# Performance work log

Measured on AMD Instinct MI355X. Metric: run time of the kernel, lower is better.

## Reference

```python
import jax, jax.numpy as jnp
import numpy as np

N_NODES = 100000
N_EDGES = 1600000
F_IN = 128
HIDDEN = [128, 128]
F_OUT = 64


def _glorot(key, shape):
    fan_in, fan_out = shape[1], shape[0]
    lim = jnp.sqrt(6.0 / (fan_in + fan_out))
    return jax.random.uniform(key, shape, jnp.float32, -lim, lim)


def setup_inputs() -> dict:
    key = jax.random.key(0)
    ks = jax.random.split(key, 12)
    x = jax.random.normal(ks[0], (N_NODES, F_IN), jnp.float32)
    edge_index = jax.random.randint(ks[1], (2, N_EDGES), 0, N_NODES, jnp.int64)
    dims = [F_IN] + HIDDEN + [F_OUT]  # [128, 128, 128, 64]
    inp = {"x": x, "edge_index": edge_index}
    for i in range(3):
        din, dout = dims[i], dims[i + 1]
        inp[f"Wl{i}"] = _glorot(ks[2 + 3 * i], (dout, din))  # neighbor lin (lin_l)
        inp[f"Wr{i}"] = _glorot(ks[3 + 3 * i], (dout, din))  # root lin (lin_r)
        inp[f"b{i}"] = jnp.zeros((dout,), jnp.float32)
    return inp


def sage_conv(x, src, dst, Wl, Wr, b):
    # PyG SAGEConv, aggr='mean': out = lin_l(mean_{j in N(i)} x_j) + lin_r(x_i) + bias
    msg = x[src]  # [E, Fin] gather from source nodes
    agg = jax.ops.segment_sum(msg, dst, num_segments=N_NODES)  # [N, Fin]
    deg = jax.ops.segment_sum(jnp.ones((src.shape[0],), x.dtype), dst,
                              num_segments=N_NODES)  # [N]
    mean = agg / jnp.maximum(deg, 1.0)[:, None]
    return mean @ Wl.T + x @ Wr.T + b


def reference(x, edge_index, Wl0, Wr0, b0, Wl1, Wr1, b1, Wl2, Wr2, b2):
    src, dst = edge_index[0], edge_index[1]
    h = jax.nn.relu(sage_conv(x, src, dst, Wl0, Wr0, b0))
    h = jax.nn.relu(sage_conv(h, src, dst, Wl1, Wr1, b1))
    out = sage_conv(h, src, dst, Wl2, Wr2, b2)  # final_conv: no relu
    return out
```

## Files before the change

kernel.cpp:

```cpp
#include <hip/hip_runtime.h>

#define NF 128
#define CHUNK 8192

typedef __attribute__((ext_vector_type(8))) short bf16x8;
typedef __attribute__((ext_vector_type(4))) float f32x4;
typedef __attribute__((ext_vector_type(2))) float f32x2;

__device__ __forceinline__ unsigned short f2b(float f) {
    unsigned int u = __float_as_uint(f);
    unsigned int r = (u + 0x7fffu + ((u >> 16) & 1u)) >> 16;
    return (unsigned short)r;
}

__device__ __forceinline__ void gld_lds16(const void* g, const void* l) {
    __builtin_amdgcn_global_load_lds(
        (const __attribute__((address_space(1))) unsigned int*)(unsigned long long)g,
        (__attribute__((address_space(3))) unsigned int*)(unsigned int)(unsigned long long)l,
        16, 0, 0);
}


__global__ __launch_bounds__(256) void prep_kernel(
        const float* __restrict__ x, unsigned short* __restrict__ xb,
        unsigned char* __restrict__ x8, int n4,
        const float* __restrict__ Wl0, const float* __restrict__ Wr0, unsigned short* __restrict__ Wc0,
        const float* __restrict__ Wl1, const float* __restrict__ Wr1, unsigned short* __restrict__ Wc1,
        const float* __restrict__ Wl2, const float* __restrict__ Wr2, const float* __restrict__ b2,
        unsigned short* __restrict__ Wst, float* __restrict__ bst,
        const int* __restrict__ dst, int* __restrict__ hist, int E, int NB,
        int bCvt, int bW0, int bW1, int bWs) {
    __shared__ int hsh[512];
    const int blk = blockIdx.x;
    const int tid = threadIdx.x;
    if (blk < bCvt) {
        int i = blk * 256 + tid;
        if (i < n4) {
            float4 v = *(const float4*)&x[(size_t)i * 4];
            uint2 o;
            o.x = (unsigned int)f2b(v.x) | ((unsigned int)f2b(v.y) << 16);
            o.y = (unsigned int)f2b(v.z) | ((unsigned int)f2b(v.w) << 16);
            *(uint2*)&xb[(size_t)i * 4] = o;
            unsigned p = __builtin_amdgcn_cvt_pk_fp8_f32(v.x, v.y, 0, false);
            p = __builtin_amdgcn_cvt_pk_fp8_f32(v.z, v.w, p, true);
            *(unsigned int*)&x8[(size_t)i * 4] = p;
        }
    } else if (blk < bW1) {
        const bool first = blk < bW0;
        int i = (blk - (first ? bCvt : bW0)) * 256 + tid;
        const float* Wl = first ? Wl0 : Wl1;
        const float* Wr = first ? Wr0 : Wr1;
        unsigned short* Wc = first ? Wc0 : Wc1;
        int f = i >> 7, k = i & 127;
        Wc[f * 256 + k] = f2b(Wl[i]);
        Wc[f * 256 + 128 + k] = f2b(Wr[i]);
    } else if (blk < bWs) {
        int i = (blk - bW1) * 256 + tid;
        int f = i >> 7, k = i & 127;
        Wst[f * 128 + k] = f2b(Wl2[i]);
        Wst[(f + 64) * 128 + k] = f2b(Wr2[i]);
        if (k == 0) {
            bst[f] = 0.f;
            bst[f + 64] = b2[f];
        }
    } else {
        const int hb = blk - bWs;
        for (int i = tid; i < NB; i += 256) hsh[i] = 0;
        __syncthreads();
        const int e0 = hb * CHUNK;
        for (int i = tid; i < CHUNK; i += 256) {
            int e = e0 + i;
            if (e < E) atomicAdd(&hsh[dst[e] >> 8], 1);
        }
        __syncthreads();
        for (int i = tid; i < NB; i += 256) hist[hb * NB + i] = hsh[i];
    }
}


__global__ __launch_bounds__(256) void sb_sum(const int* __restrict__ hist,
                                              int* __restrict__ bsum,
                                              int T, int NB, int NBLK) {
    int i = blockIdx.x * 256 + threadIdx.x;
    int v = 0;
    if (i < T) {
        int b = i / NBLK, blk = i - b * NBLK;
        v = hist[blk * NB + b];
    }
#pragma unroll
    for (int d = 32; d; d >>= 1) v += __shfl_down(v, d, 64);
    __shared__ int wsum[4];
    if ((threadIdx.x & 63) == 0) wsum[threadIdx.x >> 6] = v;
    __syncthreads();
    if (threadIdx.x == 0) bsum[blockIdx.x] = wsum[0] + wsum[1] + wsum[2] + wsum[3];
}

__global__ __launch_bounds__(1024) void sb_scan(const int* __restrict__ bsum,
                                                int* __restrict__ bpre, int NS) {
    __shared__ int s[1024];
    int t = threadIdx.x;
    int v = (t < NS) ? bsum[t] : 0;
    s[t] = v;
    __syncthreads();
    for (int d = 1; d < 1024; d <<= 1) {
        int u = (t >= d) ? s[t - d] : 0;
        __syncthreads();
        s[t] += u;
        __syncthreads();
    }
    if (t < NS) bpre[t] = s[t] - v;
}

__global__ __launch_bounds__(256) void sb_apply(const int* __restrict__ hist,
                                                const int* __restrict__ bpre,
                                                int* __restrict__ base,
                                                int* __restrict__ bstart,
                                                int T, int NB, int NBLK, int E) {
    __shared__ int s[256];
    int i = blockIdx.x * 256 + threadIdx.x;
    int t = threadIdx.x;
    int v = 0;
    int b = 0, blk = 0;
    if (i < T) {
        b = i / NBLK;
        blk = i - b * NBLK;
        v = hist[blk * NB + b];
    }
    s[t] = v;
    __syncthreads();
    for (int d = 1; d < 256; d <<= 1) {
        int u = (t >= d) ? s[t - d] : 0;
        __syncthreads();
        s[t] += u;
        __syncthreads();
    }
    if (i < T) {
        int val = bpre[blockIdx.x] + s[t] - v;
        base[i] = val;
        if (blk == 0) bstart[b] = val;
        if (i == 0) bstart[NB] = E;
    }
}

__global__ __launch_bounds__(256) void scat_kernel(const int* __restrict__ src,
                                                   const int* __restrict__ dst,
                                                   const int* __restrict__ base,
                                                   unsigned int* __restrict__ recs,
                                                   int E, int NB, int NBLK) {
    __shared__ int cur[512];
    const int blk = blockIdx.x;
    for (int b = threadIdx.x; b < NB; b += 256) cur[b] = base[b * NBLK + blk];
    __syncthreads();
    const int e0 = blk * CHUNK;
    for (int i = threadIdx.x; i < CHUNK; i += 256) {
        int e = e0 + i;
        if (e >= E) continue;
        int d = dst[e];
        int b = d >> 8;
        int pos = atomicAdd(&cur[b], 1);
        recs[pos] = (unsigned int)src[e] | ((unsigned int)(d & 255) << 24);
    }
}

__global__ __launch_bounds__(256) void csr_kernel(const unsigned int* __restrict__ recs,
                                                  const int* __restrict__ bstart,
                                                  int* __restrict__ offs,
                                                  float* __restrict__ rdeg,
                                                  int* __restrict__ csr,
                                                  int N, int E) {
    __shared__ int cnt[256];
    __shared__ int sc[256];
    __shared__ int cur[256];
    const int b = blockIdx.x;
    const int t = threadIdx.x;
    const int s0 = bstart[b], s1 = bstart[b + 1];
    cnt[t] = 0;
    __syncthreads();
    for (int i = s0 + t; i < s1; i += 256) atomicAdd(&cnt[recs[i] >> 24], 1);
    __syncthreads();
    int v = cnt[t];
    sc[t] = v;
    __syncthreads();
    for (int d = 1; d < 256; d <<= 1) {
        int u = (t >= d) ? sc[t - d] : 0;
        __syncthreads();
        sc[t] += u;
        __syncthreads();
    }
    int excl = sc[t] - v;
    int node = b * 256 + t;
    if (node < N) {
        offs[node] = s0 + excl;
        rdeg[node] = 1.0f / (float)(v > 1 ? v : 1);
        if (node == N - 1) offs[N] = E;
    }
    cur[t] = s0 + excl;
    __syncthreads();
    for (int i = s0 + t; i < s1; i += 256) {
        unsigned int r = recs[i];
        int pos = atomicAdd(&cur[r >> 24], 1);
        csr[pos] = (int)(r & 0xFFFFFFu);
    }
}


__global__ __launch_bounds__(256) void agg8_kernel(
        const unsigned char* __restrict__ h8, const int* __restrict__ offs,
        const int* __restrict__ csr, const float* __restrict__ rdeg,
        unsigned short* __restrict__ meanout, int N) {
    const int node = blockIdx.x * 4 + (threadIdx.x >> 6);
    const int lane = threadIdx.x & 63;
    if (node >= N) return;
    const int s0 = offs[node], s1 = offs[node + 1];
    const char* __restrict__ hb = (const char*)h8;
    const unsigned lane2 = (unsigned)lane * 2u;
    f32x2 acc = {0.f, 0.f};
    for (int base = s0; base < s1; base += 64) {
        const int cnt = min(64, s1 - base);
        const int boff = csr[base + min(lane, cnt - 1)] << 7;
        int j = 0;
#define AGG8_GROUP(NG)                                                         \
        {                                                                      \
            unsigned o[NG];                                                    \
            _Pragma("unroll")                                                  \
            for (int k = 0; k < NG; ++k)                                       \
                o[k] = (unsigned)__shfl(boff, j + k, 64) + lane2;              \
            unsigned int v[NG];                                                \
            _Pragma("unroll")                                                  \
            for (int k = 0; k < NG; ++k)                                       \
                v[k] = *(const unsigned short*)(hb + o[k]);                    \
            _Pragma("unroll")                                                  \
            for (int k = 0; k < NG; ++k)                                       \
                acc += __builtin_amdgcn_cvt_pk_f32_fp8(v[k], false);           \
            j += NG;                                                           \
        }
        while (j + 16 <= cnt) AGG8_GROUP(16)
        if (cnt & 8) AGG8_GROUP(8)
        if (cnt & 4) AGG8_GROUP(4)
        if (cnt & 2) AGG8_GROUP(2)
        if (cnt & 1) AGG8_GROUP(1)
#undef AGG8_GROUP
    }
    float r = rdeg[node];
    unsigned int o = (unsigned int)f2b(acc.x * r) | ((unsigned int)f2b(acc.y * r) << 16);
    *(unsigned int*)&meanout[(size_t)node * NF + lane * 2] = o;
}


__global__ __launch_bounds__(256) void agg2_kernel(
        const unsigned short* __restrict__ z, const int* __restrict__ offs,
        const int* __restrict__ csr, const float* __restrict__ rdeg,
        float* __restrict__ out, int N) {
    const int node = blockIdx.x * 4 + (threadIdx.x >> 6);
    const int lane = threadIdx.x & 63;
    if (node >= N) return;
    const int s0 = offs[node], s1 = offs[node + 1];
    const char* __restrict__ zb = (const char*)z;
    const unsigned lane2 = (unsigned)lane * 2u;
    float acc = 0.f;
    for (int base = s0; base < s1; base += 64) {
        const int cnt = min(64, s1 - base);
        const int boff = csr[base + min(lane, cnt - 1)] << 8;
        int j = 0;
#define AGG2_GROUP(NG)                                                         \
        {                                                                      \
            unsigned o[NG];                                                    \
            _Pragma("unroll")                                                  \
            for (int k = 0; k < NG; ++k)                                       \
                o[k] = (unsigned)__shfl(boff, j + k, 64) + lane2;              \
            unsigned int v[NG];                                                \
            _Pragma("unroll")                                                  \
            for (int k = 0; k < NG; ++k)                                       \
                v[k] = *(const unsigned short*)(zb + o[k]);                    \
            _Pragma("unroll")                                                  \
            for (int k = 0; k < NG; ++k)                                       \
                acc += __uint_as_float(v[k] << 16);                            \
            j += NG;                                                           \
        }
        while (j + 16 <= cnt) AGG2_GROUP(16)
        if (cnt & 8) AGG2_GROUP(8)
        if (cnt & 4) AGG2_GROUP(4)
        if (cnt & 2) AGG2_GROUP(2)
        if (cnt & 1) AGG2_GROUP(1)
#undef AGG2_GROUP
    }
    float r = rdeg[node];
    unsigned int vr = *(const unsigned short*)(zb + (size_t)node * 256 + 128 + lane2);
    out[(size_t)node * 64 + lane] = acc * r + __uint_as_float(vr << 16);
}


template <bool OUT8>
__global__ __launch_bounds__(256) void gemm_kernel(
        const unsigned short* __restrict__ Abuf,
        const unsigned short* __restrict__ Hbuf,
        const unsigned short* __restrict__ Wcat,
        const float* __restrict__ bias,
        unsigned short* __restrict__ outb,
        unsigned char* __restrict__ out8,
        int N) {
    __shared__ unsigned short As[64 * 256];

    const int tid = threadIdx.x, wid = tid >> 6, lane = tid & 63;
    const int m0 = blockIdx.x * 64;
    char* Ac = (char*)As;
    const char* Ab = (const char*)Abuf;
    const char* Hb = (const char*)Hbuf;
    const char* Wb = (const char*)Wcat;

#pragma unroll
    for (int i = 0; i < 8; ++i) {
        int off = wid * 8192 + i * 1024 + lane * 16;
        int row = off >> 9, c = off & 511;
        int c2 = c ^ ((row & 7) << 4);
        const char* srcp = (c2 < 256) ? (Ab + (size_t)(m0 + row) * 256 + c2)
                                      : (Hb + (size_t)(m0 + row) * 256 + (c2 - 256));
        gld_lds16(srcp, Ac + wid * 8192 + i * 1024);
    }
    asm volatile("s_waitcnt vmcnt(0)" ::: "memory");
    __syncthreads();

    constexpr int MI = 2;
    constexpr int NI = 4;
    const int lm = lane & 15, ko = lane >> 4;
    const int wmBase = (wid >> 1) * 32;
    const int wnBase = (wid & 1) * 64;

    f32x4 acc[MI][NI];
#pragma unroll
    for (int i = 0; i < MI; ++i)
#pragma unroll
        for (int j = 0; j < NI; ++j)
            acc[i][j] = (f32x4){0.f, 0.f, 0.f, 0.f};

#pragma unroll
    for (int ks = 0; ks < 8; ++ks) {
        const int kb = ks * 64 + ko * 16;
        bf16x8 a[MI], b[NI];
#pragma unroll
        for (int j = 0; j < NI; ++j) {
            int row = wnBase + j * 16 + lm;
            b[j] = *(const bf16x8*)(Wb + row * 512 + kb);
        }
#pragma unroll
        for (int i = 0; i < MI; ++i) {
            int row = wmBase + i * 16 + lm;
            a[i] = *(const bf16x8*)(Ac + row * 512 + (kb ^ ((row & 7) << 4)));
        }
#pragma unroll
        for (int i = 0; i < MI; ++i)
#pragma unroll
            for (int j = 0; j < NI; ++j)
                acc[i][j] = __builtin_amdgcn_mfma_f32_16x16x32_bf16(b[j], a[i], acc[i][j], 0, 0, 0);
    }

#pragma unroll
    for (int i = 0; i < MI; ++i) {
        const int node = m0 + wmBase + i * 16 + lm;
        if (node < N) {
#pragma unroll
            for (int j = 0; j < NI; ++j) {
                const int col0 = wnBase + j * 16 + ko * 4;
                const float4 bv = *(const float4*)&bias[col0];
                float v0 = fmaxf(acc[i][j][0] + bv.x, 0.f);
                float v1 = fmaxf(acc[i][j][1] + bv.y, 0.f);
                float v2 = fmaxf(acc[i][j][2] + bv.z, 0.f);
                float v3 = fmaxf(acc[i][j][3] + bv.w, 0.f);
                uint2 o;
                o.x = (unsigned int)f2b(v0) | ((unsigned int)f2b(v1) << 16);
                o.y = (unsigned int)f2b(v2) | ((unsigned int)f2b(v3) << 16);
                *(uint2*)&outb[(size_t)node * 128 + col0] = o;
                if (OUT8) {
                    unsigned p = __builtin_amdgcn_cvt_pk_fp8_f32(v0, v1, 0, false);
                    p = __builtin_amdgcn_cvt_pk_fp8_f32(v2, v3, p, true);
                    *(unsigned int*)&out8[(size_t)node * 128 + col0] = p;
                }
            }
        }
    }
}


__global__ __launch_bounds__(256) void gemmz_kernel(
        const unsigned short* __restrict__ A,
        const unsigned short* __restrict__ W,
        const float* __restrict__ bias,
        unsigned short* __restrict__ outb,
        int N) {
    __shared__ unsigned short As[64 * 128];

    const int tid = threadIdx.x, wid = tid >> 6, lane = tid & 63;
    const int m0 = blockIdx.x * 64;
    char* Ac = (char*)As;
    const char* Ab = (const char*)A;
    const char* Wb = (const char*)W;

#pragma unroll
    for (int i = 0; i < 4; ++i) {
        int off = wid * 4096 + i * 1024 + lane * 16;
        int row = off >> 8, c = off & 255;
        int c2 = c ^ ((row & 7) << 4);
        gld_lds16(Ab + (size_t)(m0 + row) * 256 + c2, Ac + wid * 4096 + i * 1024);
    }
    asm volatile("s_waitcnt vmcnt(0)" ::: "memory");
    __syncthreads();

    constexpr int MI = 2;
    constexpr int NI = 4;
    const int lm = lane & 15, ko = lane >> 4;
    const int wmBase = (wid >> 1) * 32;
    const int wnBase = (wid & 1) * 64;

    f32x4 acc[MI][NI];
#pragma unroll
    for (int i = 0; i < MI; ++i)
#pragma unroll
        for (int j = 0; j < NI; ++j)
            acc[i][j] = (f32x4){0.f, 0.f, 0.f, 0.f};

#pragma unroll
    for (int ks = 0; ks < 4; ++ks) {
        const int kb = ks * 64 + ko * 16;
        bf16x8 a[MI], b[NI];
#pragma unroll
        for (int j = 0; j < NI; ++j) {
            int row = wnBase + j * 16 + lm;
            b[j] = *(const bf16x8*)(Wb + row * 256 + kb);
        }
#pragma unroll
        for (int i = 0; i < MI; ++i) {
            int row = wmBase + i * 16 + lm;
            a[i] = *(const bf16x8*)(Ac + row * 256 + (kb ^ ((row & 7) << 4)));
        }
#pragma unroll
        for (int i = 0; i < MI; ++i)
#pragma unroll
            for (int j = 0; j < NI; ++j)
                acc[i][j] = __builtin_amdgcn_mfma_f32_16x16x32_bf16(b[j], a[i], acc[i][j], 0, 0, 0);
    }

#pragma unroll
    for (int i = 0; i < MI; ++i) {
        const int node = m0 + wmBase + i * 16 + lm;
        if (node < N) {
#pragma unroll
            for (int j = 0; j < NI; ++j) {
                const int col0 = wnBase + j * 16 + ko * 4;
                const float4 bv = *(const float4*)&bias[col0];
                uint2 o;
                o.x = (unsigned int)f2b(acc[i][j][0] + bv.x) |
                      ((unsigned int)f2b(acc[i][j][1] + bv.y) << 16);
                o.y = (unsigned int)f2b(acc[i][j][2] + bv.z) |
                      ((unsigned int)f2b(acc[i][j][3] + bv.w) << 16);
                *(uint2*)&outb[(size_t)node * 128 + col0] = o;
            }
        }
    }
}


extern "C" void kernel_launch(void* const* d_in, const int* in_sizes, int n_in,
                              void* d_out, int out_size, void* d_ws, size_t ws_size,
                              hipStream_t stream) {
    const float* x   = (const float*)d_in[0];
    const int*   ei  = (const int*)d_in[1];
    const float* Wl0 = (const float*)d_in[2];
    const float* Wr0 = (const float*)d_in[3];
    const float* b0  = (const float*)d_in[4];
    const float* Wl1 = (const float*)d_in[5];
    const float* Wr1 = (const float*)d_in[6];
    const float* b1  = (const float*)d_in[7];
    const float* Wl2 = (const float*)d_in[8];
    const float* Wr2 = (const float*)d_in[9];
    const float* b2  = (const float*)d_in[10];
    float* out = (float*)d_out;

    const int N = in_sizes[0] / NF;
    const int E = in_sizes[1] / 2;
    const int* srcv = ei;
    const int* dstv = ei + E;

    const int NB   = (N + 255) >> 8;
    const int NBLK = (E + CHUNK - 1) / CHUNK;
    const int T    = NB * NBLK;
    const int NS   = (T + 255) / 256;

    char* w = (char*)d_ws;
    auto alloc = [&](size_t bytes) {
        void* p = (void*)w;
        w += (bytes + 255) & ~(size_t)255;
        return p;
    };
    unsigned short* xb   = (unsigned short*)alloc((size_t)N * NF * 2);
    unsigned short* h1b  = (unsigned short*)alloc((size_t)N * NF * 2);
    unsigned short* h2b  = (unsigned short*)alloc((size_t)N * NF * 2);
    unsigned short* mb   = (unsigned short*)alloc((size_t)N * NF * 2);
    unsigned char*  u8   = (unsigned char*)alloc((size_t)N * NF * 2);
    unsigned char*  x8   = u8;
    unsigned char*  h18  = u8 + (size_t)N * NF;
    unsigned short* z2b  = (unsigned short*)u8;
    unsigned short* Wc0  = (unsigned short*)alloc((size_t)128 * 256 * 2);
    unsigned short* Wc1  = (unsigned short*)alloc((size_t)128 * 256 * 2);
    unsigned short* Wst2 = (unsigned short*)alloc((size_t)128 * 128 * 2);
    float*          bst2 = (float*)alloc((size_t)128 * 4);
    int*   offs   = (int*)alloc((size_t)(N + 1) * 4);
    int*   csr    = (int*)alloc((size_t)E * 4);
    float* rdeg   = (float*)alloc((size_t)N * 4);
    unsigned int* recs = (unsigned int*)alloc((size_t)E * 4);
    int*   hist   = (int*)alloc((size_t)T * 4);
    int*   base   = (int*)alloc((size_t)T * 4);
    int*   bstart = (int*)alloc((size_t)(NB + 1) * 4);
    int*   sb1    = (int*)alloc((size_t)1024 * 4);
    int*   sb2    = (int*)alloc((size_t)1024 * 4);

    const int n4 = N * NF / 4;
    const int bCvt = (n4 + 255) / 256;
    const int bW0  = bCvt + 64;
    const int bW1  = bW0 + 64;
    const int bWs  = bW1 + 32;
    const int bTot = bWs + NBLK;

    prep_kernel<<<bTot, 256, 0, stream>>>(x, xb, x8, n4,
                                          Wl0, Wr0, Wc0, Wl1, Wr1, Wc1,
                                          Wl2, Wr2, b2, Wst2, bst2,
                                          dstv, hist, E, NB,
                                          bCvt, bW0, bW1, bWs);
    sb_sum<<<NS, 256, 0, stream>>>(hist, sb1, T, NB, NBLK);
    sb_scan<<<1, 1024, 0, stream>>>(sb1, sb2, NS);
    sb_apply<<<NS, 256, 0, stream>>>(hist, sb2, base, bstart, T, NB, NBLK, E);
    scat_kernel<<<NBLK, 256, 0, stream>>>(srcv, dstv, base, recs, E, NB, NBLK);
    csr_kernel<<<NB, 256, 0, stream>>>(recs, bstart, offs, rdeg, csr, N, E);

    const int ab = (N + 3) / 4;
    const int gb = (N + 63) / 64;

    agg8_kernel<<<ab, 256, 0, stream>>>(x8, offs, csr, rdeg, mb, N);
    gemm_kernel<true><<<gb, 256, 0, stream>>>(mb, xb, Wc0, b0, h1b, h18, N);

    agg8_kernel<<<ab, 256, 0, stream>>>(h18, offs, csr, rdeg, mb, N);
    gemm_kernel<false><<<gb, 256, 0, stream>>>(mb, h1b, Wc1, b1, h2b, nullptr, N);

    gemmz_kernel<<<gb, 256, 0, stream>>>(h2b, Wst2, bst2, z2b, N);
    agg2_kernel<<<ab, 256, 0, stream>>>(z2b, offs, csr, rdeg, out, N);
}
```

Before: 306.6 us.

## Fuse mean aggregation into the layer GEMM via shared-memory tiles

Measured after the change: 346.0 us. 1.13x slower.

```diff
diff --git a/kernel.cpp b/kernel.cpp
--- a/kernel.cpp
+++ b/kernel.cpp
@@ -204,46 +204,139 @@
 }
 
 
-__global__ __launch_bounds__(256) void agg8_kernel(
-        const unsigned char* __restrict__ h8, const int* __restrict__ offs,
-        const int* __restrict__ csr, const float* __restrict__ rdeg,
-        unsigned short* __restrict__ meanout, int N) {
-    const int node = blockIdx.x * 4 + (threadIdx.x >> 6);
-    const int lane = threadIdx.x & 63;
-    if (node >= N) return;
-    const int s0 = offs[node], s1 = offs[node + 1];
-    const char* __restrict__ hb = (const char*)h8;
+template <bool OUT8>
+__global__ __launch_bounds__(256) void fused_layer(
+        const unsigned char* __restrict__ g8,
+        const unsigned short* __restrict__ root,
+        const int* __restrict__ offs, const int* __restrict__ csr,
+        const float* __restrict__ rdeg,
+        const unsigned short* __restrict__ Wcat,
+        const float* __restrict__ bias,
+        unsigned short* __restrict__ outb,
+        unsigned char* __restrict__ out8,
+        int N) {
+    __shared__ unsigned short Am[64 * 128];
+    __shared__ unsigned short Ar[64 * 128];
+
+    const int tid = threadIdx.x, wid = tid >> 6, lane = tid & 63;
+    const int m0 = blockIdx.x * 64;
+    char* Amc = (char*)Am;
+    char* Arc = (char*)Ar;
+    const char* Rb = (const char*)root;
+    const char* Wb = (const char*)Wcat;
+
+#pragma unroll
+    for (int i = 0; i < 4; ++i) {
+        int off = wid * 4096 + i * 1024 + lane * 16;
+        int row = off >> 8, c = off & 255;
+        int c2 = c ^ ((row & 7) << 4);
+        gld_lds16(Rb + (size_t)(m0 + row) * 256 + c2, Arc + wid * 4096 + i * 1024);
+    }
+
+    const char* __restrict__ hb = (const char*)g8;
     const unsigned lane2 = (unsigned)lane * 2u;
-    f32x2 acc = {0.f, 0.f};
-    for (int base = s0; base < s1; base += 64) {
-        const int cnt = min(64, s1 - base);
-        const int boff = csr[base + min(lane, cnt - 1)] << 7;
-        int j = 0;
+    for (int t = 0; t < 16; ++t) {
+        const int node = m0 + wid * 16 + t;
+        if (node >= N) break;
+        const int s0 = offs[node], s1 = offs[node + 1];
+        f32x2 acc = {0.f, 0.f};
+        for (int base = s0; base < s1; base += 64) {
+            const int cnt = min(64, s1 - base);
+            const int boff = csr[base + min(lane, cnt - 1)] << 7;
+            int j = 0;
 #define AGG8_GROUP(NG)                                                         \
-        {                                                                      \
-            unsigned o[NG];                                                    \
-            _Pragma("unroll")                                                  \
-            for (int k = 0; k < NG; ++k)                                       \
-                o[k] = (unsigned)__shfl(boff, j + k, 64) + lane2;              \
-            unsigned int v[NG];                                                \
-            _Pragma("unroll")                                                  \
-            for (int k = 0; k < NG; ++k)                                       \
-                v[k] = *(const unsigned short*)(hb + o[k]);                    \
-            _Pragma("unroll")                                                  \
-            for (int k = 0; k < NG; ++k)                                       \
-                acc += __builtin_amdgcn_cvt_pk_f32_fp8(v[k], false);           \
-            j += NG;                                                           \
-        }
-        while (j + 16 <= cnt) AGG8_GROUP(16)
-        if (cnt & 8) AGG8_GROUP(8)
-        if (cnt & 4) AGG8_GROUP(4)
-        if (cnt & 2) AGG8_GROUP(2)
-        if (cnt & 1) AGG8_GROUP(1)
+            {                                                                  \
+                unsigned o[NG];                                                \
+                _Pragma("unroll")                                              \
+                for (int k = 0; k < NG; ++k)                                   \
+                    o[k] = (unsigned)__shfl(boff, j + k, 64) + lane2;          \
+                unsigned int v[NG];                                            \
+                _Pragma("unroll")                                              \
+                for (int k = 0; k < NG; ++k)                                   \
+                    v[k] = *(const unsigned short*)(hb + o[k]);                \
+                _Pragma("unroll")                                              \
+                for (int k = 0; k < NG; ++k)                                   \
+                    acc += __builtin_amdgcn_cvt_pk_f32_fp8(v[k], false);       \
+                j += NG;                                                       \
+            }
+            while (j + 16 <= cnt) AGG8_GROUP(16)
+            if (cnt & 8) AGG8_GROUP(8)
+            if (cnt & 4) AGG8_GROUP(4)
+            if (cnt & 2) AGG8_GROUP(2)
+            if (cnt & 1) AGG8_GROUP(1)
 #undef AGG8_GROUP
-    }
-    float r = rdeg[node];
-    unsigned int o = (unsigned int)f2b(acc.x * r) | ((unsigned int)f2b(acc.y * r) << 16);
-    *(unsigned int*)&meanout[(size_t)node * NF + lane * 2] = o;
+        }
+        const float r = rdeg[node];
+        const unsigned int mo = (unsigned int)f2b(acc.x * r) |
+                                ((unsigned int)f2b(acc.y * r) << 16);
+        const int lrow = wid * 16 + t;
+        const unsigned doff = (unsigned)lrow * 256 +
+                              (((unsigned)lane * 4u) ^ (((unsigned)(lrow & 7)) << 4));
+        *(unsigned int*)(Amc + doff) = mo;
+    }
+    asm volatile("s_waitcnt vmcnt(0)" ::: "memory");
+    __syncthreads();
+
+    constexpr int MI = 2;
+    constexpr int NI = 4;
+    const int lm = lane & 15, ko = lane >> 4;
+    const int wmBase = (wid >> 1) * 32;
+    const int wnBase = (wid & 1) * 64;
+
+    f32x4 acc[MI][NI];
+#pragma unroll
+    for (int i = 0; i < MI; ++i)
+#pragma unroll
+        for (int j = 0; j < NI; ++j)
+            acc[i][j] = (f32x4){0.f, 0.f, 0.f, 0.f};
+
+#pragma unroll
+    for (int ks = 0; ks < 8; ++ks) {
+        const int kb = ks * 64 + ko * 16;
+        const int kbl = kb & 255;
+        const char* Abase = (ks < 4) ? Amc : Arc;
+        bf16x8 a[MI], b[NI];
+#pragma unroll
+        for (int j = 0; j < NI; ++j) {
+            int row = wnBase + j * 16 + lm;
+            b[j] = *(const bf16x8*)(Wb + row * 512 + kb);
+        }
+#pragma unroll
+        for (int i = 0; i < MI; ++i) {
+            int row = wmBase + i * 16 + lm;
+            a[i] = *(const bf16x8*)(Abase + row * 256 + (kbl ^ ((row & 7) << 4)));
+        }
+#pragma unroll
+        for (int i = 0; i < MI; ++i)
+#pragma unroll
+            for (int j = 0; j < NI; ++j)
+                acc[i][j] = __builtin_amdgcn_mfma_f32_16x16x32_bf16(b[j], a[i], acc[i][j], 0, 0, 0);
+    }
+
+#pragma unroll
+    for (int i = 0; i < MI; ++i) {
+        const int node = m0 + wmBase + i * 16 + lm;
+        if (node < N) {
+#pragma unroll
+            for (int j = 0; j < NI; ++j) {
+                const int col0 = wnBase + j * 16 + ko * 4;
+                const float4 bv = *(const float4*)&bias[col0];
+                float v0 = fmaxf(acc[i][j][0] + bv.x, 0.f);
+                float v1 = fmaxf(acc[i][j][1] + bv.y, 0.f);
+                float v2 = fmaxf(acc[i][j][2] + bv.z, 0.f);
+                float v3 = fmaxf(acc[i][j][3] + bv.w, 0.f);
+                uint2 o;
+                o.x = (unsigned int)f2b(v0) | ((unsigned int)f2b(v1) << 16);
+                o.y = (unsigned int)f2b(v2) | ((unsigned int)f2b(v3) << 16);
+                *(uint2*)&outb[(size_t)node * 128 + col0] = o;
+                if (OUT8) {
+                    unsigned p = __builtin_amdgcn_cvt_pk_fp8_f32(v0, v1, 0, false);
+                    p = __builtin_amdgcn_cvt_pk_fp8_f32(v2, v3, p, true);
+                    *(unsigned int*)&out8[(size_t)node * 128 + col0] = p;
+                }
+            }
+        }
+    }
 }
 
 
@@ -290,97 +383,6 @@
 }
 
 
-template <bool OUT8>
-__global__ __launch_bounds__(256) void gemm_kernel(
-        const unsigned short* __restrict__ Abuf,
-        const unsigned short* __restrict__ Hbuf,
-        const unsigned short* __restrict__ Wcat,
-        const float* __restrict__ bias,
-        unsigned short* __restrict__ outb,
-        unsigned char* __restrict__ out8,
-        int N) {
-    __shared__ unsigned short As[64 * 256];
-
-    const int tid = threadIdx.x, wid = tid >> 6, lane = tid & 63;
-    const int m0 = blockIdx.x * 64;
-    char* Ac = (char*)As;
-    const char* Ab = (const char*)Abuf;
-    const char* Hb = (const char*)Hbuf;
-    const char* Wb = (const char*)Wcat;
-
-#pragma unroll
-    for (int i = 0; i < 8; ++i) {
-        int off = wid * 8192 + i * 1024 + lane * 16;
-        int row = off >> 9, c = off & 511;
-        int c2 = c ^ ((row & 7) << 4);
-        const char* srcp = (c2 < 256) ? (Ab + (size_t)(m0 + row) * 256 + c2)
-                                      : (Hb + (size_t)(m0 + row) * 256 + (c2 - 256));
-        gld_lds16(srcp, Ac + wid * 8192 + i * 1024);
-    }
-    asm volatile("s_waitcnt vmcnt(0)" ::: "memory");
-    __syncthreads();
-
-    constexpr int MI = 2;
-    constexpr int NI = 4;
-    const int lm = lane & 15, ko = lane >> 4;
-    const int wmBase = (wid >> 1) * 32;
-    const int wnBase = (wid & 1) * 64;
-
-    f32x4 acc[MI][NI];
-#pragma unroll
-    for (int i = 0; i < MI; ++i)
-#pragma unroll
-        for (int j = 0; j < NI; ++j)
-            acc[i][j] = (f32x4){0.f, 0.f, 0.f, 0.f};
-
-#pragma unroll
-    for (int ks = 0; ks < 8; ++ks) {
-        const int kb = ks * 64 + ko * 16;
-        bf16x8 a[MI], b[NI];
-#pragma unroll
-        for (int j = 0; j < NI; ++j) {
-            int row = wnBase + j * 16 + lm;
-            b[j] = *(const bf16x8*)(Wb + row * 512 + kb);
-        }
-#pragma unroll
-        for (int i = 0; i < MI; ++i) {
-            int row = wmBase + i * 16 + lm;
-            a[i] = *(const bf16x8*)(Ac + row * 512 + (kb ^ ((row & 7) << 4)));
-        }
-#pragma unroll
-        for (int i = 0; i < MI; ++i)
-#pragma unroll
-            for (int j = 0; j < NI; ++j)
-                acc[i][j] = __builtin_amdgcn_mfma_f32_16x16x32_bf16(b[j], a[i], acc[i][j], 0, 0, 0);
-    }
-
-#pragma unroll
-    for (int i = 0; i < MI; ++i) {
-        const int node = m0 + wmBase + i * 16 + lm;
-        if (node < N) {
-#pragma unroll
-            for (int j = 0; j < NI; ++j) {
-                const int col0 = wnBase + j * 16 + ko * 4;
-                const float4 bv = *(const float4*)&bias[col0];
-                float v0 = fmaxf(acc[i][j][0] + bv.x, 0.f);
-                float v1 = fmaxf(acc[i][j][1] + bv.y, 0.f);
-                float v2 = fmaxf(acc[i][j][2] + bv.z, 0.f);
-                float v3 = fmaxf(acc[i][j][3] + bv.w, 0.f);
-                uint2 o;
-                o.x = (unsigned int)f2b(v0) | ((unsigned int)f2b(v1) << 16);
-                o.y = (unsigned int)f2b(v2) | ((unsigned int)f2b(v3) << 16);
-                *(uint2*)&outb[(size_t)node * 128 + col0] = o;
-                if (OUT8) {
-                    unsigned p = __builtin_amdgcn_cvt_pk_fp8_f32(v0, v1, 0, false);
-                    p = __builtin_amdgcn_cvt_pk_fp8_f32(v2, v3, p, true);
-                    *(unsigned int*)&out8[(size_t)node * 128 + col0] = p;
-                }
-            }
-        }
-    }
-}
-
-
 __global__ __launch_bounds__(256) void gemmz_kernel(
         const unsigned short* __restrict__ A,
         const unsigned short* __restrict__ W,
@@ -494,7 +496,6 @@
     unsigned short* xb   = (unsigned short*)alloc((size_t)N * NF * 2);
     unsigned short* h1b  = (unsigned short*)alloc((size_t)N * NF * 2);
     unsigned short* h2b  = (unsigned short*)alloc((size_t)N * NF * 2);
-    unsigned short* mb   = (unsigned short*)alloc((size_t)N * NF * 2);
     unsigned char*  u8   = (unsigned char*)alloc((size_t)N * NF * 2);
     unsigned char*  x8   = u8;
     unsigned char*  h18  = u8 + (size_t)N * NF;
@@ -531,15 +532,15 @@
     scat_kernel<<<NBLK, 256, 0, stream>>>(srcv, dstv, base, recs, E, NB, NBLK);
     csr_kernel<<<NB, 256, 0, stream>>>(recs, bstart, offs, rdeg, csr, N, E);
 
-    const int ab = (N + 3) / 4;
-    const int gb = (N + 63) / 64;
-
-    agg8_kernel<<<ab, 256, 0, stream>>>(x8, offs, csr, rdeg, mb, N);
-    gemm_kernel<true><<<gb, 256, 0, stream>>>(mb, xb, Wc0, b0, h1b, h18, N);
-
-    agg8_kernel<<<ab, 256, 0, stream>>>(h18, offs, csr, rdeg, mb, N);
-    gemm_kernel<false><<<gb, 256, 0, stream>>>(mb, h1b, Wc1, b1, h2b, nullptr, N);
-
-    gemmz_kernel<<<gb, 256, 0, stream>>>(h2b, Wst2, bst2, z2b, N);
+    const int ab  = (N + 3) / 4;
+    const int gb64 = (N + 63) / 64;
+
+    fused_layer<true><<<gb64, 256, 0, stream>>>(x8, xb, offs, csr, rdeg,
+                                                Wc0, b0, h1b, h18, N);
+
+    fused_layer<false><<<gb64, 256, 0, stream>>>(h18, h1b, offs, csr, rdeg,
+                                                 Wc1, b1, h2b, nullptr, N);
+
+    gemmz_kernel<<<gb64, 256, 0, stream>>>(h2b, Wst2, bst2, z2b, N);
     agg2_kernel<<<ab, 256, 0, stream>>>(z2b, offs, csr, rdeg, out, N);
 }
```

## Load GEMM A operands directly from global memory and double rows per block

Applied to the files above, without the earlier changes.

Measured after the change: 319.4 us. +4.2%, slower.

```diff
diff --git a/kernel.cpp b/kernel.cpp
--- a/kernel.cpp
+++ b/kernel.cpp
@@ -11,13 +11,6 @@
     unsigned int u = __float_as_uint(f);
     unsigned int r = (u + 0x7fffu + ((u >> 16) & 1u)) >> 16;
     return (unsigned short)r;
-}
-
-__device__ __forceinline__ void gld_lds16(const void* g, const void* l) {
-    __builtin_amdgcn_global_load_lds(
-        (const __attribute__((address_space(1))) unsigned int*)(unsigned long long)g,
-        (__attribute__((address_space(3))) unsigned int*)(unsigned int)(unsigned long long)l,
-        16, 0, 0);
 }
 
 
@@ -299,32 +292,25 @@
         unsigned short* __restrict__ outb,
         unsigned char* __restrict__ out8,
         int N) {
-    __shared__ unsigned short As[64 * 256];
-
     const int tid = threadIdx.x, wid = tid >> 6, lane = tid & 63;
-    const int m0 = blockIdx.x * 64;
-    char* Ac = (char*)As;
-    const char* Ab = (const char*)Abuf;
-    const char* Hb = (const char*)Hbuf;
-    const char* Wb = (const char*)Wcat;
-
-#pragma unroll
-    for (int i = 0; i < 8; ++i) {
-        int off = wid * 8192 + i * 1024 + lane * 16;
-        int row = off >> 9, c = off & 511;
-        int c2 = c ^ ((row & 7) << 4);
-        const char* srcp = (c2 < 256) ? (Ab + (size_t)(m0 + row) * 256 + c2)
-                                      : (Hb + (size_t)(m0 + row) * 256 + (c2 - 256));
-        gld_lds16(srcp, Ac + wid * 8192 + i * 1024);
-    }
-    asm volatile("s_waitcnt vmcnt(0)" ::: "memory");
-    __syncthreads();
-
-    constexpr int MI = 2;
+    const int m0 = blockIdx.x * 128;
+    const int lm = lane & 15, ko = lane >> 4;
+    const int wmBase = (wid >> 1) * 64;
+    const int wnBase = (wid & 1) * 64;
+    const char* __restrict__ Ab = (const char*)Abuf;
+    const char* __restrict__ Hb = (const char*)Hbuf;
+    const char* __restrict__ Wb = (const char*)Wcat;
+
+    constexpr int MI = 4;
     constexpr int NI = 4;
-    const int lm = lane & 15, ko = lane >> 4;
-    const int wmBase = (wid >> 1) * 32;
-    const int wnBase = (wid & 1) * 64;
+
+    size_t arow[MI];
+#pragma unroll
+    for (int i = 0; i < MI; ++i)
+        arow[i] = (size_t)min(m0 + wmBase + i * 16 + lm, N - 1) * 256;
+    const size_t wrow[NI] = {
+        (size_t)(wnBase + 0 * 16 + lm) * 512, (size_t)(wnBase + 1 * 16 + lm) * 512,
+        (size_t)(wnBase + 2 * 16 + lm) * 512, (size_t)(wnBase + 3 * 16 + lm) * 512};
 
     f32x4 acc[MI][NI];
 #pragma unroll
@@ -336,17 +322,15 @@
 #pragma unroll
     for (int ks = 0; ks < 8; ++ks) {
         const int kb = ks * 64 + ko * 16;
+        const int kbl = kb & 255;
+        const char* __restrict__ Abase = (ks < 4) ? Ab : Hb;
         bf16x8 a[MI], b[NI];
 #pragma unroll
-        for (int j = 0; j < NI; ++j) {
-            int row = wnBase + j * 16 + lm;
-            b[j] = *(const bf16x8*)(Wb + row * 512 + kb);
-        }
-#pragma unroll
-        for (int i = 0; i < MI; ++i) {
-            int row = wmBase + i * 16 + lm;
-            a[i] = *(const bf16x8*)(Ac + row * 512 + (kb ^ ((row & 7) << 4)));
-        }
+        for (int j = 0; j < NI; ++j)
+            b[j] = *(const bf16x8*)(Wb + wrow[j] + kb);
+#pragma unroll
+        for (int i = 0; i < MI; ++i)
+            a[i] = *(const bf16x8*)(Abase + arow[i] + kbl);
 #pragma unroll
         for (int i = 0; i < MI; ++i)
 #pragma unroll
@@ -387,64 +371,52 @@
         const float* __restrict__ bias,
         unsigned short* __restrict__ outb,
         int N) {
-    __shared__ unsigned short As[64 * 128];
-
     const int tid = threadIdx.x, wid = tid >> 6, lane = tid & 63;
-    const int m0 = blockIdx.x * 64;
-    char* Ac = (char*)As;
-    const char* Ab = (const char*)A;
-    const char* Wb = (const char*)W;
-
-#pragma unroll
-    for (int i = 0; i < 4; ++i) {
-        int off = wid * 4096 + i * 1024 + lane * 16;
-        int row = off >> 8, c = off & 255;
-        int c2 = c ^ ((row & 7) << 4);
-        gld_lds16(Ab + (size_t)(m0 + row) * 256 + c2, Ac + wid * 4096 + i * 1024);
-    }
-    asm volatile("s_waitcnt vmcnt(0)" ::: "memory");
-    __syncthreads();
-
-    constexpr int MI = 2;
-    constexpr int NI = 4;
+    const int m0 = blockIdx.x * 128;
     const int lm = lane & 15, ko = lane >> 4;
-    const int wmBase = (wid >> 1) * 32;
+    const int wmBase = (wid >> 1) * 64;
     const int wnBase = (wid & 1) * 64;
-
-    f32x4 acc[MI][NI];
-#pragma unroll
-    for (int i = 0; i < MI; ++i)
-#pragma unroll
-        for (int j = 0; j < NI; ++j)
+    const char* __restrict__ Ab = (const char*)A;
+    const char* __restrict__ Wb = (const char*)W;
+
+    size_t arow[4];
+#pragma unroll
+    for (int i = 0; i < 4; ++i)
+        arow[i] = (size_t)min(m0 + wmBase + i * 16 + lm, N - 1) * 256;
+    const size_t wrow[4] = {
+        (size_t)(wnBase + 0 * 16 + lm) * 256, (size_t)(wnBase + 1 * 16 + lm) * 256,
+        (size_t)(wnBase + 2 * 16 + lm) * 256, (size_t)(wnBase + 3 * 16 + lm) * 256};
+
+    f32x4 acc[4][4];
+#pragma unroll
+    for (int i = 0; i < 4; ++i)
+#pragma unroll
+        for (int j = 0; j < 4; ++j)
             acc[i][j] = (f32x4){0.f, 0.f, 0.f, 0.f};
 
 #pragma unroll
     for (int ks = 0; ks < 4; ++ks) {
         const int kb = ks * 64 + ko * 16;
-        bf16x8 a[MI], b[NI];
-#pragma unroll
-        for (int j = 0; j < NI; ++j) {
-            int row = wnBase + j * 16 + lm;
-            b[j] = *(const bf16x8*)(Wb + row * 256 + kb);
-        }
-#pragma unroll
-        for (int i = 0; i < MI; ++i) {
-            int row = wmBase + i * 16 + lm;
-            a[i] = *(const bf16x8*)(Ac + row * 256 + (kb ^ ((row & 7) << 4)));
-        }
-#pragma unroll
-        for (int i = 0; i < MI; ++i)
-#pragma unroll
-            for (int j = 0; j < NI; ++j)
+        bf16x8 a[4], b[4];
+#pragma unroll
+        for (int j = 0; j < 4; ++j)
+            b[j] = *(const bf16x8*)(Wb + wrow[j] + kb);
+#pragma unroll
+        for (int i = 0; i < 4; ++i)
+            a[i] = *(const bf16x8*)(Ab + arow[i] + kb);
+#pragma unroll
+        for (int i = 0; i < 4; ++i)
+#pragma unroll
+            for (int j = 0; j < 4; ++j)
                 acc[i][j] = __builtin_amdgcn_mfma_f32_16x16x32_bf16(b[j], a[i], acc[i][j], 0, 0, 0);
     }
 
 #pragma unroll
-    for (int i = 0; i < MI; ++i) {
+    for (int i = 0; i < 4; ++i) {
         const int node = m0 + wmBase + i * 16 + lm;
         if (node < N) {
 #pragma unroll
-            for (int j = 0; j < NI; ++j) {
+            for (int j = 0; j < 4; ++j) {
                 const int col0 = wnBase + j * 16 + ko * 4;
                 const float4 bv = *(const float4*)&bias[col0];
                 uint2 o;
@@ -531,8 +503,8 @@
     scat_kernel<<<NBLK, 256, 0, stream>>>(srcv, dstv, base, recs, E, NB, NBLK);
     csr_kernel<<<NB, 256, 0, stream>>>(recs, bstart, offs, rdeg, csr, N, E);
 
-    const int ab = (N + 3) / 4;
-    const int gb = (N + 63) / 64;
+    const int ab  = (N + 3) / 4;
+    const int gb  = (N + 127) / 128;
 
     agg8_kernel<<<ab, 256, 0, stream>>>(x8, offs, csr, rdeg, mb, N);
     gemm_kernel<true><<<gb, 256, 0, stream>>>(mb, xb, Wc0, b0, h1b, h18, N);
```
